# Performance work log

Hardware: AMD Instinct MI355X
Metric: run time of the kernel (lower is better)

## Reference

```python
import jax, jax.numpy as jnp
import numpy as np

B, N, DIM = 2, 2048, 1024
HEADS, DIM_HEAD = 16, 64
INNER = HEADS * DIM_HEAD  # 1024
SCALE = DIM_HEAD ** -0.5


def setup_inputs() -> dict:
    key = jax.random.key(0)
    ks = jax.random.split(key, 6)
    s = lambda k, shape, fan: jax.random.normal(k, shape, jnp.float32) * (fan ** -0.5)
    return {
        "x": jax.random.normal(ks[0], (B, N, DIM), jnp.float32),
        "similarity": jax.random.normal(ks[1], (B, N), jnp.float32),
        "Wq": s(ks[2], (DIM, INNER), DIM),
        "Wkv": s(ks[3], (DIM, 2 * INNER), DIM),
        "Wo": s(ks[4], (INNER, DIM), INNER),
        "bo": jnp.zeros((DIM,), jnp.float32),
    }


def reference(x, similarity, Wq, Wkv, Wo, bo):
    b, n, _ = x.shape
    h, d = HEADS, DIM_HEAD
    # projections (context = x, self-attention)
    q = (x @ Wq).reshape(b, n, h, d).transpose(0, 2, 1, 3)        # b h n d
    kv = x @ Wkv                                                   # b n 2*inner
    k, v = jnp.split(kv, 2, axis=-1)
    k = k.reshape(b, n, h, d).transpose(0, 2, 1, 3)
    v = v.reshape(b, n, h, d).transpose(0, 2, 1, 3)
    dots = jnp.einsum('bhid,bhjd->bhij', q, k) * SCALE             # b h n n
    # similarity [b,n] -> broadcast as per-query row bias [b,1,n,1]
    dots = dots + similarity[:, None, :, None]
    attn = jax.nn.softmax(dots, axis=-1)
    out = jnp.einsum('bhij,bhjd->bhid', attn, v)                   # b h n d
    out = out.transpose(0, 2, 1, 3).reshape(b, n, h * d)           # b n inner
    return out @ Wo + bo
```

## Files before the change

### kernel.cpp

```cpp
#include <hip/hip_runtime.h>


typedef __attribute__((ext_vector_type(8))) short short8;
typedef __attribute__((ext_vector_type(4))) float float4_;
typedef __attribute__((ext_vector_type(16))) float floatx16;
typedef __attribute__((ext_vector_type(4))) unsigned short ushort4_;
typedef __attribute__((ext_vector_type(2))) unsigned int uint2_;
typedef __attribute__((ext_vector_type(4))) unsigned int uint4_;

#define MFMA(a, b, c) __builtin_amdgcn_mfma_f32_16x16x32_bf16((a), (b), (c), 0, 0, 0)
#define MFMA32(a, b, c) __builtin_amdgcn_mfma_f32_32x32x16_bf16((a), (b), (c), 0, 0, 0)

static __device__ __forceinline__ unsigned short f2bf(float f) {
    union { float f; unsigned int u; } v; v.f = f;
    unsigned int r = v.u + 0x7FFFu + ((v.u >> 16) & 1u);
    return (unsigned short)(r >> 16);
}

static __device__ __forceinline__ void gld16(const void* g, void* l) {
    __builtin_amdgcn_global_load_lds(
        (__attribute__((address_space(1))) void*)(g),
        (__attribute__((address_space(3))) void*)(l), 16, 0, 0);
}

__global__ __launch_bounds__(256) void prep(
    const float* __restrict__ X, const float* __restrict__ Wq,
    const float* __restrict__ Wkv, const float* __restrict__ Wo,
    unsigned short* __restrict__ xb, unsigned short* __restrict__ Wt,
    unsigned short* __restrict__ Wot)
{
    const int bid = blockIdx.x, t = threadIdx.x;
    if (bid >= 1024) {
        const int b = bid - 1024;
        const float4_* src = (const float4_*)X;
        ushort4_* dst = (ushort4_*)xb;
        #pragma unroll
        for (int g = 0; g < 8; ++g) {
            const int idx = b * 2048 + g * 256 + t;
            float4_ v = src[idx];
            ushort4_ o;
            o[0] = f2bf(v[0]); o[1] = f2bf(v[1]);
            o[2] = f2bf(v[2]); o[3] = f2bf(v[3]);
            dst[idx] = o;
        }
        return;
    }
    __shared__ float tile[64][65];
    const float* src; unsigned short* dst; int N, kt, nt, drow0;
    if (bid < 256)      { src = Wq;  N = 1024; kt = bid & 15;       nt = bid >> 4;       dst = Wt;  drow0 = nt * 64; }
    else if (bid < 768) { src = Wkv; N = 2048; kt = (bid-256) & 15; nt = (bid-256) >> 4; dst = Wt;  drow0 = 1024 + nt * 64; }
    else                { src = Wo;  N = 1024; kt = (bid-768) & 15; nt = (bid-768) >> 4; dst = Wot; drow0 = nt * 64; }
    const int k0 = kt * 64, n0 = nt * 64;
    const int r0 = t >> 6, c = t & 63;
    #pragma unroll
    for (int i = 0; i < 16; ++i) {
        const int r = i * 4 + r0;
        tile[r][c] = src[(size_t)(k0 + r) * N + n0 + c];
    }
    __syncthreads();
    #pragma unroll
    for (int i = 0; i < 16; ++i) {
        const int rn = i * 4 + r0;
        dst[(size_t)(drow0 + rn) * 1024 + k0 + c] = f2bf(tile[c][rn]);
    }
}

__global__ __launch_bounds__(256) void qkv_gemm2(
    const unsigned short* __restrict__ xb, const unsigned short* __restrict__ Wt,
    unsigned short* __restrict__ q_ws, unsigned short* __restrict__ k_ws,
    unsigned short* __restrict__ vt_ws)
{
    __shared__ unsigned short As[128 * 64];
    __shared__ unsigned short Bs[128 * 64];
    const int t = threadIdx.x, wave = t >> 6, lane = t & 63;
    const int L = lane & 15, quad = lane >> 4;
    const int mb = blockIdx.x / 24, nb = blockIdx.x % 24;
    const int m0 = mb * 128, n0 = nb * 128;
    const int wr = wave >> 1, wc = wave & 1;

    float4_ z = {0.f, 0.f, 0.f, 0.f};
    float4_ acc[4][4];
    #pragma unroll
    for (int i = 0; i < 4; ++i)
        #pragma unroll
        for (int j = 0; j < 4; ++j) acc[i][j] = z;

    const unsigned short* gA[4]; const unsigned short* gB[4];
    unsigned short* lA[4]; unsigned short* lB[4];
    #pragma unroll
    for (int j = 0; j < 4; ++j) {
        const int cid = wave * 256 + j * 64 + lane;
        const int row = cid >> 3, pc = cid & 7;
        const int lch = pc ^ (row & 7);
        gA[j] = xb + (size_t)(m0 + row) * 1024 + lch * 8;
        gB[j] = Wt + (size_t)(n0 + row) * 1024 + lch * 8;
        lA[j] = As + wave * 2048 + j * 512;
        lB[j] = Bs + wave * 2048 + j * 512;
    }

    for (int kc = 0; kc < 1024; kc += 64) {
        #pragma unroll
        for (int j = 0; j < 4; ++j) {
            gld16(gA[j] + kc, lA[j]);
            gld16(gB[j] + kc, lB[j]);
        }
        __syncthreads();
        #pragma unroll
        for (int ks = 0; ks < 2; ++ks) {
            short8 af[4], bfr[4];
            #pragma unroll
            for (int mt = 0; mt < 4; ++mt) {
                const int rl = wr * 64 + mt * 16 + L;
                af[mt] = *(const short8*)(As + rl * 64 + (((ks * 4 + quad) ^ (L & 7)) << 3));
            }
            #pragma unroll
            for (int nt = 0; nt < 4; ++nt) {
                const int rl = wc * 64 + nt * 16 + L;
                bfr[nt] = *(const short8*)(Bs + rl * 64 + (((ks * 4 + quad) ^ (L & 7)) << 3));
            }
            #pragma unroll
            for (int mt = 0; mt < 4; ++mt)
                #pragma unroll
                for (int nt = 0; nt < 4; ++nt)
                    acc[mt][nt] = MFMA(af[mt], bfr[nt], acc[mt][nt]);
        }
        __syncthreads();
    }

    const int b = m0 >> 11;
    const int type = n0 >> 10;
    #pragma unroll
    for (int mt = 0; mt < 4; ++mt) {
        const int m = (m0 & 2047) + wr * 64 + mt * 16 + quad * 4;
        #pragma unroll
        for (int nt = 0; nt < 4; ++nt) {
            const int cl = (n0 & 1023) + wc * 64 + nt * 16 + L;
            const int h = cl >> 6, d = cl & 63;
            float4_ v = acc[mt][nt];
            if (type == 0) {
                unsigned short* p = q_ws + ((size_t)(b * 16 + h) * 2048 + m) * 64 + d;
                #pragma unroll
                for (int r = 0; r < 4; ++r) p[(size_t)r * 64] = f2bf(v[r] * 0.18033688011f);
            } else if (type == 1) {
                unsigned short* p = k_ws + ((size_t)(b * 16 + h) * 2048 + m) * 64 + d;
                #pragma unroll
                for (int r = 0; r < 4; ++r) p[(size_t)r * 64] = f2bf(v[r]);
            } else {
                ushort4_ pk;
                pk[0] = f2bf(v[0]); pk[1] = f2bf(v[1]);
                pk[2] = f2bf(v[2]); pk[3] = f2bf(v[3]);
                *(ushort4_*)(vt_ws + ((size_t)(b * 16 + h) * 64 + d) * 2048 + m) = pk;
            }
        }
    }
}

__global__ __launch_bounds__(256) void attn_fwd3(
    const unsigned short* __restrict__ q_ws,
    const unsigned short* __restrict__ k_ws,
    const unsigned short* __restrict__ vt_ws,
    unsigned short* __restrict__ o2)
{
    __shared__ unsigned short k_lds[2][64 * 64];
    __shared__ unsigned short v_lds[2][64 * 64];
    __shared__ float ls[4][32];
    const int t = threadIdx.x, wave = t >> 6, lane = t & 63;
    const int l32 = lane & 31, hi = lane >> 5;
    const int xcd = blockIdx.x & 7, loc = blockIdx.x >> 3;
    const int bh = xcd * 4 + (loc >> 4);
    const int qb = loc & 15;

    const unsigned short* Kp = k_ws + (size_t)bh * 2048 * 64;
    const unsigned short* Vt = vt_ws + (size_t)bh * 64 * 2048;

    const unsigned short* Qp = q_ws + ((size_t)bh * 2048 + qb * 128 + wave * 32 + l32) * 64;
    short8 qf[4];
    #pragma unroll
    for (int s = 0; s < 4; ++s) qf[s] = *(const short8*)(Qp + hi * 8 + s * 16);

    const int c0 = wave * 64 + lane;
    const int kr0 = c0 >> 3, kl0 = (c0 & 7) ^ (kr0 & 7);
    const int kr1 = kr0 + 32;
    const unsigned short* ks0 = Kp + (size_t)kr0 * 64 + kl0 * 8;
    const unsigned short* ks1 = Kp + (size_t)kr1 * 64 + kl0 * 8;
    const unsigned short* vs0 = Vt + (size_t)kr0 * 2048 + kl0 * 8;
    const unsigned short* vs1 = Vt + (size_t)kr1 * 2048 + kl0 * 8;
    const int dst0 = wave * 512, dst1 = 2048 + wave * 512;

    floatx16 o0, o1;
    #pragma unroll
    for (int r = 0; r < 16; ++r) { o0[r] = 0.f; o1[r] = 0.f; }
    float lsum = 0.f;

    gld16(ks0, k_lds[0] + dst0); gld16(ks1, k_lds[0] + dst1);
    gld16(vs0, v_lds[0] + dst0); gld16(vs1, v_lds[0] + dst1);
    __syncthreads();

    const int sw = l32 & 7;
    for (int j0 = 0; j0 < 2048; j0 += 64) {
        const int p = (j0 >> 6) & 1;
        if (j0 + 64 < 2048) {
            const int np = p ^ 1;
            gld16(ks0 + (j0 + 64) * 64, k_lds[np] + dst0);
            gld16(ks1 + (j0 + 64) * 64, k_lds[np] + dst1);
            gld16(vs0 + (j0 + 64), v_lds[np] + dst0);
            gld16(vs1 + (j0 + 64), v_lds[np] + dst1);
        }
        const unsigned short* kb = k_lds[p];
        const unsigned short* vb = v_lds[p];

        floatx16 s0, s1;
        #pragma unroll
        for (int r = 0; r < 16; ++r) { s0[r] = 0.f; s1[r] = 0.f; }
        #pragma unroll
        for (int s = 0; s < 4; ++s) {
            const int lch = 2 * s + hi;
            short8 k0 = *(const short8*)(kb + l32 * 64 + ((lch ^ sw) << 3));
            short8 k1 = *(const short8*)(kb + (32 + l32) * 64 + ((lch ^ sw) << 3));
            s0 = MFMA32(k0, qf[s], s0);
            s1 = MFMA32(k1, qf[s], s1);
        }

        unsigned int pk0[8], pk1[8];
        #pragma unroll
        for (int d = 0; d < 8; ++d) {
            union { float f; unsigned int u; } a0, b0, a1, b1;
            a0.f = __builtin_amdgcn_exp2f(s0[2 * d]);
            b0.f = __builtin_amdgcn_exp2f(s0[2 * d + 1]);
            a1.f = __builtin_amdgcn_exp2f(s1[2 * d]);
            b1.f = __builtin_amdgcn_exp2f(s1[2 * d + 1]);
            lsum += (a0.f + b0.f) + (a1.f + b1.f);
            pk0[d] = (a0.u >> 16) | (b0.u & 0xFFFF0000u);
            pk1[d] = (a1.u >> 16) | (b1.u & 0xFFFF0000u);
        }

        #pragma unroll
        for (int w = 0; w < 4; ++w) {
            uint4_ pw;
            if (w == 0)      { pw[0] = pk0[0]; pw[1] = pk0[1]; pw[2] = pk0[2]; pw[3] = pk0[3]; }
            else if (w == 1) { pw[0] = pk0[4]; pw[1] = pk0[5]; pw[2] = pk0[6]; pw[3] = pk0[7]; }
            else if (w == 2) { pw[0] = pk1[0]; pw[1] = pk1[1]; pw[2] = pk1[2]; pw[3] = pk1[3]; }
            else             { pw[0] = pk1[4]; pw[1] = pk1[5]; pw[2] = pk1[6]; pw[3] = pk1[7]; }
            short8 pa = *(short8*)&pw;

            const unsigned short* vr0 = vb + l32 * 64;
            const unsigned short* vr1 = vb + (32 + l32) * 64;
            const int ca = (((2 * w) ^ sw) << 3) + 4 * hi;
            const int cb = (((2 * w + 1) ^ sw) << 3) + 4 * hi;
            uint2_ va0 = *(const uint2_*)(vr0 + ca);
            uint2_ vb0 = *(const uint2_*)(vr0 + cb);
            uint2_ va1 = *(const uint2_*)(vr1 + ca);
            uint2_ vb1 = *(const uint2_*)(vr1 + cb);
            uint4_ f0, f1;
            f0[0] = va0[0]; f0[1] = va0[1]; f0[2] = vb0[0]; f0[3] = vb0[1];
            f1[0] = va1[0]; f1[1] = va1[1]; f1[2] = vb1[0]; f1[3] = vb1[1];
            o0 = MFMA32(pa, *(short8*)&f0, o0);
            o1 = MFMA32(pa, *(short8*)&f1, o1);
        }
        __syncthreads();
    }

    float ltot = lsum + __shfl_xor(lsum, 32);
    ls[wave][l32] = ltot;
    float inv[16];
    #pragma unroll
    for (int r = 0; r < 16; ++r)
        inv[r] = 1.0f / ls[wave][(r & 3) + 8 * (r >> 2) + 4 * hi];

    const int b = bh >> 4, h = bh & 15;
    unsigned short* ob = o2 + ((size_t)b * 2048 + qb * 128 + wave * 32) * 1024 + h * 64;
    #pragma unroll
    for (int r = 0; r < 16; ++r) {
        const int row = (r & 3) + 8 * (r >> 2) + 4 * hi;
        ob[(size_t)row * 1024 + l32]      = f2bf(o0[r] * inv[r]);
        ob[(size_t)row * 1024 + 32 + l32] = f2bf(o1[r] * inv[r]);
    }
}

__global__ __launch_bounds__(256) void out_gemm2(
    const unsigned short* __restrict__ o2, const unsigned short* __restrict__ Wot,
    const float* __restrict__ bo, float* __restrict__ Out)
{
    __shared__ unsigned short As[128 * 64];
    __shared__ unsigned short Bs[64 * 64];
    const int t = threadIdx.x, wave = t >> 6, lane = t & 63;
    const int L = lane & 15, quad = lane >> 4;
    const int mb = blockIdx.x >> 4, nb = blockIdx.x & 15;
    const int m0 = mb * 128, n0 = nb * 64;
    const int wr = wave >> 1, wc = wave & 1;

    float4_ z = {0.f, 0.f, 0.f, 0.f};
    float4_ acc[4][2];
    #pragma unroll
    for (int i = 0; i < 4; ++i)
        #pragma unroll
        for (int j = 0; j < 2; ++j) acc[i][j] = z;

    const unsigned short* gA[4]; unsigned short* lA[4];
    #pragma unroll
    for (int j = 0; j < 4; ++j) {
        const int cid = wave * 256 + j * 64 + lane;
        const int row = cid >> 3, pc = cid & 7;
        gA[j] = o2 + (size_t)(m0 + row) * 1024 + (pc ^ (row & 7)) * 8;
        lA[j] = As + wave * 2048 + j * 512;
    }
    const unsigned short* gB[2]; unsigned short* lB[2];
    #pragma unroll
    for (int j = 0; j < 2; ++j) {
        const int cid = wave * 128 + j * 64 + lane;
        const int row = cid >> 3, pc = cid & 7;
        gB[j] = Wot + (size_t)(n0 + row) * 1024 + (pc ^ (row & 7)) * 8;
        lB[j] = Bs + wave * 1024 + j * 512;
    }

    for (int kc = 0; kc < 1024; kc += 64) {
        #pragma unroll
        for (int j = 0; j < 4; ++j) gld16(gA[j] + kc, lA[j]);
        #pragma unroll
        for (int j = 0; j < 2; ++j) gld16(gB[j] + kc, lB[j]);
        __syncthreads();
        #pragma unroll
        for (int ks = 0; ks < 2; ++ks) {
            short8 af[4], bfr[2];
            #pragma unroll
            for (int mt = 0; mt < 4; ++mt) {
                const int rl = wr * 64 + mt * 16 + L;
                af[mt] = *(const short8*)(As + rl * 64 + (((ks * 4 + quad) ^ (L & 7)) << 3));
            }
            #pragma unroll
            for (int nt = 0; nt < 2; ++nt) {
                const int rl = wc * 32 + nt * 16 + L;
                bfr[nt] = *(const short8*)(Bs + rl * 64 + (((ks * 4 + quad) ^ (L & 7)) << 3));
            }
            #pragma unroll
            for (int mt = 0; mt < 4; ++mt)
                #pragma unroll
                for (int nt = 0; nt < 2; ++nt)
                    acc[mt][nt] = MFMA(af[mt], bfr[nt], acc[mt][nt]);
        }
        __syncthreads();
    }

    #pragma unroll
    for (int mt = 0; mt < 4; ++mt) {
        const int m = m0 + wr * 64 + mt * 16 + quad * 4;
        #pragma unroll
        for (int nt = 0; nt < 2; ++nt) {
            const int c = n0 + wc * 32 + nt * 16 + L;
            const float bias = bo[c];
            #pragma unroll
            for (int r = 0; r < 4; ++r)
                Out[(size_t)(m + r) * 1024 + c] = acc[mt][nt][r] + bias;
        }
    }
}

extern "C" void kernel_launch(void* const* d_in, const int* in_sizes, int n_in,
                              void* d_out, int out_size, void* d_ws, size_t ws_size,
                              hipStream_t stream) {
    const float* x   = (const float*)d_in[0];
    const float* Wq  = (const float*)d_in[2];
    const float* Wkv = (const float*)d_in[3];
    const float* Wo  = (const float*)d_in[4];
    const float* bo  = (const float*)d_in[5];
    float* out = (float*)d_out;

    char* ws = (char*)d_ws;
    const size_t MB = 1024 * 1024;
    unsigned short* xb   = (unsigned short*)(ws);
    unsigned short* o2   = xb;
    unsigned short* Wt   = (unsigned short*)(ws + 8 * MB);
    unsigned short* Wot  = (unsigned short*)(ws + 14 * MB);
    unsigned short* q_ws = (unsigned short*)(ws + 16 * MB);
    unsigned short* k_ws = (unsigned short*)(ws + 24 * MB);
    unsigned short* vt_ws= (unsigned short*)(ws + 32 * MB);

    prep<<<dim3(1536), dim3(256), 0, stream>>>(x, Wq, Wkv, Wo, xb, Wt, Wot);
    qkv_gemm2<<<dim3(768), dim3(256), 0, stream>>>(xb, Wt, q_ws, k_ws, vt_ws);
    attn_fwd3<<<dim3(512), dim3(256), 0, stream>>>(q_ws, k_ws, vt_ws, o2);
    out_gemm2<<<dim3(512), dim3(256), 0, stream>>>(o2, Wot, bo, out);
}
```

Before: 197.1 us.

## Permute K rows so P·V uses contiguous 16-byte LDS reads for V

```diff
diff --git a/kernel.cpp b/kernel.cpp
--- a/kernel.cpp
+++ b/kernel.cpp
@@ -5,7 +5,6 @@
 typedef __attribute__((ext_vector_type(4))) float float4_;
 typedef __attribute__((ext_vector_type(16))) float floatx16;
 typedef __attribute__((ext_vector_type(4))) unsigned short ushort4_;
-typedef __attribute__((ext_vector_type(2))) unsigned int uint2_;
 typedef __attribute__((ext_vector_type(4))) unsigned int uint4_;
 
 #define MFMA(a, b, c) __builtin_amdgcn_mfma_f32_16x16x32_bf16((a), (b), (c), 0, 0, 0)
@@ -155,7 +154,7 @@
     }
 }
 
-__global__ __launch_bounds__(256) void attn_fwd3(
+__global__ __launch_bounds__(256) void attn_fwd5(
     const unsigned short* __restrict__ q_ws,
     const unsigned short* __restrict__ k_ws,
     const unsigned short* __restrict__ vt_ws,
@@ -176,15 +175,15 @@
     const unsigned short* Qp = q_ws + ((size_t)bh * 2048 + qb * 128 + wave * 32 + l32) * 64;
     short8 qf[4];
     #pragma unroll
-    for (int s = 0; s < 4; ++s) qf[s] = *(const short8*)(Qp + hi * 8 + s * 16);
+    for (int k = 0; k < 4; ++k) qf[k] = *(const short8*)(Qp + hi * 8 + k * 16);
 
     const int c0 = wave * 64 + lane;
     const int kr0 = c0 >> 3, kl0 = (c0 & 7) ^ (kr0 & 7);
-    const int kr1 = kr0 + 32;
-    const unsigned short* ks0 = Kp + (size_t)kr0 * 64 + kl0 * 8;
-    const unsigned short* ks1 = Kp + (size_t)kr1 * 64 + kl0 * 8;
+    const int pr0 = (kr0 & ~12) | ((kr0 & 4) << 1) | ((kr0 & 8) >> 1);
+    const unsigned short* ks0 = Kp + (size_t)pr0 * 64 + kl0 * 8;
+    const unsigned short* ks1 = ks0 + 32 * 64;
     const unsigned short* vs0 = Vt + (size_t)kr0 * 2048 + kl0 * 8;
-    const unsigned short* vs1 = Vt + (size_t)kr1 * 2048 + kl0 * 8;
+    const unsigned short* vs1 = Vt + (size_t)(kr0 + 32) * 2048 + kl0 * 8;
     const int dst0 = wave * 512, dst1 = 2048 + wave * 512;
 
     floatx16 o0, o1;
@@ -197,14 +196,16 @@
     __syncthreads();
 
     const int sw = l32 & 7;
-    for (int j0 = 0; j0 < 2048; j0 += 64) {
-        const int p = (j0 >> 6) & 1;
-        if (j0 + 64 < 2048) {
+    #pragma unroll 2
+    for (int it = 0; it < 32; ++it) {
+        const int p = it & 1;
+        if (it + 1 < 32) {
             const int np = p ^ 1;
-            gld16(ks0 + (j0 + 64) * 64, k_lds[np] + dst0);
-            gld16(ks1 + (j0 + 64) * 64, k_lds[np] + dst1);
-            gld16(vs0 + (j0 + 64), v_lds[np] + dst0);
-            gld16(vs1 + (j0 + 64), v_lds[np] + dst1);
+            const int joff = (it + 1) * 64;
+            gld16(ks0 + (size_t)joff * 64, k_lds[np] + dst0);
+            gld16(ks1 + (size_t)joff * 64, k_lds[np] + dst1);
+            gld16(vs0 + joff, v_lds[np] + dst0);
+            gld16(vs1 + joff, v_lds[np] + dst1);
         }
         const unsigned short* kb = k_lds[p];
         const unsigned short* vb = v_lds[p];
@@ -213,12 +214,12 @@
         #pragma unroll
         for (int r = 0; r < 16; ++r) { s0[r] = 0.f; s1[r] = 0.f; }
         #pragma unroll
-        for (int s = 0; s < 4; ++s) {
-            const int lch = 2 * s + hi;
+        for (int k = 0; k < 4; ++k) {
+            const int lch = 2 * k + hi;
             short8 k0 = *(const short8*)(kb + l32 * 64 + ((lch ^ sw) << 3));
             short8 k1 = *(const short8*)(kb + (32 + l32) * 64 + ((lch ^ sw) << 3));
-            s0 = MFMA32(k0, qf[s], s0);
-            s1 = MFMA32(k1, qf[s], s1);
+            s0 = MFMA32(k0, qf[k], s0);
+            s1 = MFMA32(k1, qf[k], s1);
         }
 
         unsigned int pk0[8], pk1[8];
@@ -230,8 +231,8 @@
             a1.f = __builtin_amdgcn_exp2f(s1[2 * d]);
             b1.f = __builtin_amdgcn_exp2f(s1[2 * d + 1]);
             lsum += (a0.f + b0.f) + (a1.f + b1.f);
-            pk0[d] = (a0.u >> 16) | (b0.u & 0xFFFF0000u);
-            pk1[d] = (a1.u >> 16) | (b1.u & 0xFFFF0000u);
+            pk0[d] = __builtin_amdgcn_perm(b0.u, a0.u, 0x07060302u);
+            pk1[d] = __builtin_amdgcn_perm(b1.u, a1.u, 0x07060302u);
         }
 
         #pragma unroll
@@ -242,20 +243,11 @@
             else if (w == 2) { pw[0] = pk1[0]; pw[1] = pk1[1]; pw[2] = pk1[2]; pw[3] = pk1[3]; }
             else             { pw[0] = pk1[4]; pw[1] = pk1[5]; pw[2] = pk1[6]; pw[3] = pk1[7]; }
             short8 pa = *(short8*)&pw;
-
-            const unsigned short* vr0 = vb + l32 * 64;
-            const unsigned short* vr1 = vb + (32 + l32) * 64;
-            const int ca = (((2 * w) ^ sw) << 3) + 4 * hi;
-            const int cb = (((2 * w + 1) ^ sw) << 3) + 4 * hi;
-            uint2_ va0 = *(const uint2_*)(vr0 + ca);
-            uint2_ vb0 = *(const uint2_*)(vr0 + cb);
-            uint2_ va1 = *(const uint2_*)(vr1 + ca);
-            uint2_ vb1 = *(const uint2_*)(vr1 + cb);
-            uint4_ f0, f1;
-            f0[0] = va0[0]; f0[1] = va0[1]; f0[2] = vb0[0]; f0[3] = vb0[1];
-            f1[0] = va1[0]; f1[1] = va1[1]; f1[2] = vb1[0]; f1[3] = vb1[1];
-            o0 = MFMA32(pa, *(short8*)&f0, o0);
-            o1 = MFMA32(pa, *(short8*)&f1, o1);
+            const int c = 2 * w + hi;
+            short8 vf0 = *(const short8*)(vb + l32 * 64 + ((c ^ sw) << 3));
+            short8 vf1 = *(const short8*)(vb + (32 + l32) * 64 + ((c ^ sw) << 3));
+            o0 = MFMA32(pa, vf0, o0);
+            o1 = MFMA32(pa, vf1, o1);
         }
         __syncthreads();
     }
@@ -377,6 +369,6 @@
 
     prep<<<dim3(1536), dim3(256), 0, stream>>>(x, Wq, Wkv, Wo, xb, Wt, Wot);
     qkv_gemm2<<<dim3(768), dim3(256), 0, stream>>>(xb, Wt, q_ws, k_ws, vt_ws);
-    attn_fwd3<<<dim3(512), dim3(256), 0, stream>>>(q_ws, k_ws, vt_ws, o2);
+    attn_fwd5<<<dim3(512), dim3(256), 0, stream>>>(q_ws, k_ws, vt_ws, o2);
     out_gemm2<<<dim3(512), dim3(256), 0, stream>>>(o2, Wot, bo, out);
 }
```

After: 187.0 us. -5.1%, faster.
